# Performance work log

Measured on AMD Instinct MI355X. Metric: run time of the kernel, lower is better.

## Reference

```python
import jax, jax.numpy as jnp
import numpy as np

B, T, D = 8, 1024, 1024

def setup_inputs() -> dict:
    key = jax.random.key(0)
    ks = jax.random.split(key, 9)
    s = D ** -0.5
    return {
        "x": jax.random.normal(ks[0], (B, T, D), dtype=jnp.float32),
        "w_q": jax.random.normal(ks[1], (D, D), dtype=jnp.float32) * s,
        "b_q": jax.random.normal(ks[2], (D,), dtype=jnp.float32) * 0.02,
        "w_k": jax.random.normal(ks[3], (D, D), dtype=jnp.float32) * s,
        "b_k": jax.random.normal(ks[4], (D,), dtype=jnp.float32) * 0.02,
        "w_v": jax.random.normal(ks[5], (D, D), dtype=jnp.float32) * s,
        "b_v": jax.random.normal(ks[6], (D,), dtype=jnp.float32) * 0.02,
        "w_o": jax.random.normal(ks[7], (D, D), dtype=jnp.float32) * s,
        "b_o": jax.random.normal(ks[8], (D,), dtype=jnp.float32) * 0.02,
    }

def reference(x, w_q, b_q, w_k, b_k, w_v, b_v, w_o, b_o):
    d = x.shape[-1]
    scale = jnp.asarray(d, x.dtype) ** -0.5
    q = jnp.einsum('btd,ed->bte', x, w_q) + b_q  # nn.Linear: x @ W^T + b
    k = jnp.einsum('btd,ed->bte', x, w_k) + b_k
    v = jnp.einsum('btd,ed->bte', x, w_v) + b_v
    t = x.shape[1]
    causal = jnp.tril(jnp.ones((t, t), dtype=bool))  # (T, T)
    scores = jnp.einsum('bqd,bkd->bqk', q, k) * scale
    scores = jnp.where(causal, scores, -jnp.inf)
    attn = jax.nn.softmax(scores, axis=-1)  # max-subtraction folded in
    out = jnp.einsum('bqk,bkd->bqd', attn, v)
    return jnp.einsum('btd,ed->bte', out, w_o) + b_o
```

## Files before the change

### kernel.cpp

```cpp
#include <hip/hip_runtime.h>

typedef unsigned short u16;
typedef __attribute__((ext_vector_type(8))) short short8;
typedef __attribute__((ext_vector_type(4))) float f32x4;


__device__ __forceinline__ u16 f2bf(float f) {
  unsigned u = __builtin_bit_cast(unsigned, f);
  u += 0x7fffu + ((u >> 16) & 1u);
  return (u16)(u >> 16);
}

__device__ __forceinline__ void gload16(const void* g, void* l) {
  __builtin_amdgcn_global_load_lds(
      (const __attribute__((address_space(1))) unsigned*)g,
      (__attribute__((address_space(3))) unsigned*)l, 16, 0, 0);
}


#define QTILE(CUR, NXT, DOSTAGE, VM)                                         \
  {                                                                          \
    char* cA = sA0 + (CUR) * 32768;                                          \
    char* cB = sB0 + (CUR) * 16384;                                          \
    short8 bf[2][4], af[2][2];                                               \
                         \
    _Pragma("unroll") for (int kk = 0; kk < 2; ++kk)                         \
      _Pragma("unroll") for (int j = 0; j < 4; ++j) {                        \
        const int rn = wc + j * 16 + l16;                                    \
        bf[kk][j] = *(const short8*)(cB + rn * 128 + (((kk << 2) + quad) ^ (rn & 7)) * 16); \
      }                                                                      \
    _Pragma("unroll") for (int kk = 0; kk < 2; ++kk)                         \
      _Pragma("unroll") for (int i = 0; i < 2; ++i) {                        \
        const int rm = wr + i * 16 + l16;                                    \
        af[kk][i] = *(const short8*)(cA + rm * 128 + (((kk << 2) + quad) ^ (rm & 7)) * 16); \
      }                                                                      \
    if (DOSTAGE) {                                                           \
      char* dA = sA0 + (NXT) * 32768;                                        \
      _Pragma("unroll") for (int j = 0; j < 3; ++j) { gload16(ga[j], dA + la[j]); ga[j] += 64; } \
    }                                                                        \
    asm volatile("" ::: "memory");                                           \
    __builtin_amdgcn_s_barrier();                                            \
    asm volatile("s_waitcnt lgkmcnt(0)" ::: "memory");                       \
    __builtin_amdgcn_sched_barrier(0);                                       \
    __builtin_amdgcn_s_setprio(1);                                           \
    _Pragma("unroll") for (int kk = 0; kk < 2; ++kk)                         \
      _Pragma("unroll") for (int i = 0; i < 2; ++i)                          \
        _Pragma("unroll") for (int j = 0; j < 4; ++j)                        \
          acc[i][j] = __builtin_amdgcn_mfma_f32_16x16x32_bf16(af[kk][i], bf[kk][j], acc[i][j], 0, 0, 0); \
    __builtin_amdgcn_s_setprio(0);                                           \
    asm volatile("" ::: "memory");                                           \
    __builtin_amdgcn_s_barrier();                                            \
    asm volatile("" ::: "memory");                                           \
                                \
    _Pragma("unroll") for (int kk = 0; kk < 2; ++kk)                         \
      _Pragma("unroll") for (int i = 0; i < 2; ++i) {                        \
        const int rm = wr + 32 + i * 16 + l16;                               \
        af[kk][i] = *(const short8*)(cA + rm * 128 + (((kk << 2) + quad) ^ (rm & 7)) * 16); \
      }                                                                      \
    if (DOSTAGE) {                                                           \
      char* dA = sA0 + (NXT) * 32768;                                        \
      char* dB = sB0 + (NXT) * 16384;                                        \
      gload16(ga[3], dA + la[3]); ga[3] += 64;                               \
      _Pragma("unroll") for (int j = 0; j < 2; ++j) { gload16(gb[j], dB + lb[j]); gb[j] += 64; } \
    }                                                                        \
    asm volatile("s_waitcnt vmcnt(" #VM ")" ::: "memory");                   \
    asm volatile("" ::: "memory");                                           \
    __builtin_amdgcn_s_barrier();                                            \
    asm volatile("s_waitcnt lgkmcnt(0)" ::: "memory");                       \
    __builtin_amdgcn_sched_barrier(0);                                       \
    __builtin_amdgcn_s_setprio(1);                                           \
    _Pragma("unroll") for (int kk = 0; kk < 2; ++kk)                         \
      _Pragma("unroll") for (int i = 0; i < 2; ++i)                          \
        _Pragma("unroll") for (int j = 0; j < 4; ++j)                        \
          acc[2 + i][j] = __builtin_amdgcn_mfma_f32_16x16x32_bf16(af[kk][i], bf[kk][j], acc[2 + i][j], 0, 0, 0); \
    __builtin_amdgcn_s_setprio(0);                                           \
    asm volatile("" ::: "memory");                                           \
    __builtin_amdgcn_s_barrier();                                            \
    asm volatile("" ::: "memory");                                           \
  }

__device__ __forceinline__ void gemm_256x128(
    const u16* __restrict__ A, const u16* __restrict__ B,
    int m0, int n0, char* smem, f32x4 acc[4][4])
{
  const int tid  = threadIdx.x;
  const int lane = tid & 63;
  const int quad = lane >> 4;
  const int l16  = lane & 15;
  const int wave = tid >> 6;
  const int wr   = (wave >> 1) << 6;
  const int wc   = (wave & 1) << 6;

  const u16* ga[4]; int la[4];
  const u16* gb[2]; int lb[2];
#pragma unroll
  for (int j = 0; j < 4; ++j) {
    const int L = j * 512 + tid;
    const int r = L >> 3;
    const int c = (L & 7) ^ (r & 7);
    la[j] = L * 16;
    ga[j] = A + (size_t)(m0 + r) * 1024 + c * 8;
  }
#pragma unroll
  for (int j = 0; j < 2; ++j) {
    const int L = j * 512 + tid;
    const int r = L >> 3;
    const int c = (L & 7) ^ (r & 7);
    lb[j] = L * 16;
    gb[j] = B + (size_t)(n0 + r) * 1024 + c * 8;
  }
  char* const sA0 = smem;
  char* const sB0 = smem + 98304;

  {
    char* dA = sA0; char* dB = sB0;
#pragma unroll
    for (int j = 0; j < 4; ++j) { gload16(ga[j], dA + la[j]); ga[j] += 64; }
#pragma unroll
    for (int j = 0; j < 2; ++j) { gload16(gb[j], dB + lb[j]); gb[j] += 64; }
  }
  {
    char* dA = sA0 + 32768; char* dB = sB0 + 16384;
#pragma unroll
    for (int j = 0; j < 4; ++j) { gload16(ga[j], dA + la[j]); ga[j] += 64; }
#pragma unroll
    for (int j = 0; j < 2; ++j) { gload16(gb[j], dB + lb[j]); gb[j] += 64; }
  }
  asm volatile("s_waitcnt vmcnt(6)" ::: "memory");
  __builtin_amdgcn_s_barrier();
  asm volatile("" ::: "memory");

  int cur = 0;
#pragma unroll 1
  for (int t = 0; t < 14; ++t) {
    int nxt = cur + 2; if (nxt >= 3) nxt -= 3;
    QTILE(cur, nxt, true, 6);
    cur = (cur + 1 == 3) ? 0 : cur + 1;
  }
  QTILE(cur, 0, false, 0);
  cur = (cur + 1 == 3) ? 0 : cur + 1;
  QTILE(cur, 0, false, 0);
}

#define ACC_ZERO4(acc) { _Pragma("unroll") for (int i=0;i<4;++i) \
  _Pragma("unroll") for (int j=0;j<4;++j) \
  _Pragma("unroll") for (int r=0;r<4;++r) acc[i][j][r]=0.f; }
#define ACC_ZERO2(acc) { _Pragma("unroll") for (int i=0;i<2;++i) \
  _Pragma("unroll") for (int j=0;j<4;++j) \
  _Pragma("unroll") for (int r=0;r<4;++r) acc[i][j][r]=0.f; }

__device__ __forceinline__ void store256x128_bf16(
    f32x4 acc[4][4], const float* bias, int n0,
    u16* C, int m0, char* smem)
{
  const int tid = threadIdx.x, lane = tid & 63, wave = tid >> 6;
  const int quad = lane >> 4, l16 = lane & 15;
  const int wr = (wave >> 1) << 6, wc = (wave & 1) << 6;
  u16* t = (u16*)smem;
#pragma unroll
  for (int j = 0; j < 4; ++j) {
    const int nn = wc + j * 16 + l16;
    const float bj = bias[n0 + nn];
#pragma unroll
    for (int i = 0; i < 4; ++i) {
      const int mm = wr + i * 16 + quad * 4;
#pragma unroll
      for (int r = 0; r < 4; ++r)
        t[(mm + r) * 136 + nn] = f2bf(acc[i][j][r] + bj);
    }
  }
  __syncthreads();
#pragma unroll
  for (int it = 0; it < 8; ++it) {
    const int L = it * 512 + tid;
    const int mm = L >> 4, cc = L & 15;
    *(uint4*)(C + (size_t)(m0 + mm) * 1024 + n0 + cc * 8) =
        *(const uint4*)(t + mm * 136 + cc * 8);
  }
}

__device__ __forceinline__ void gemm_tile_64(
    const u16* __restrict__ A, int lda,
    const u16* __restrict__ B, int ldb,
    int m0, int n0, int kend,
    char* sA, char* sB, f32x4 acc[2][4])
{
  const int tid  = threadIdx.x;
  const int lane = tid & 63;
  const int wave = tid >> 6;
  const int quad = lane >> 4;
  const int l16  = lane & 15;
  const int wr   = (wave >> 1) << 5;
  const int wc   = (wave & 1) << 6;

  const u16* ga[2]; int la[2];
  const u16* gb[4]; int lb[4];
#pragma unroll
  for (int j = 0; j < 2; ++j) {
    const int Lb = j * 256 + wave * 64;
    const int L  = Lb + lane;
    const int r  = L >> 3;
    const int c  = (L & 7) ^ (r & 7);
    la[j] = Lb * 16;
    ga[j] = A + (size_t)(m0 + r) * lda + c * 8;
  }
#pragma unroll
  for (int j = 0; j < 4; ++j) {
    const int Lb = j * 256 + wave * 64;
    const int L  = Lb + lane;
    const int r  = L >> 3;
    const int c  = (L & 7) ^ (r & 7);
    lb[j] = Lb * 16;
    gb[j] = B + (size_t)(n0 + r) * ldb + c * 8;
  }

  for (int kt = 0; kt < kend; kt += 64) {
#pragma unroll
    for (int j = 0; j < 2; ++j) { gload16(ga[j], sA + la[j]); ga[j] += 64; }
#pragma unroll
    for (int j = 0; j < 4; ++j) { gload16(gb[j], sB + lb[j]); gb[j] += 64; }
    __syncthreads();
#pragma unroll
    for (int kk = 0; kk < 2; ++kk) {
      short8 af[2], bfr[4];
#pragma unroll
      for (int i = 0; i < 2; ++i) {
        const int rm = wr + i * 16 + l16;
        af[i] = *(const short8*)(sA + rm * 128 + (((kk << 2) + quad) ^ (rm & 7)) * 16);
      }
#pragma unroll
      for (int j = 0; j < 4; ++j) {
        const int rn = wc + j * 16 + l16;
        bfr[j] = *(const short8*)(sB + rn * 128 + (((kk << 2) + quad) ^ (rn & 7)) * 16);
      }
#pragma unroll
      for (int i = 0; i < 2; ++i)
#pragma unroll
        for (int j = 0; j < 4; ++j)
          acc[i][j] = __builtin_amdgcn_mfma_f32_16x16x32_bf16(af[i], bfr[j], acc[i][j], 0, 0, 0);
    }
    __syncthreads();
  }
}

__global__ __launch_bounds__(256) void cast_inputs(
    const float* __restrict__ x,  const float* __restrict__ wq,
    const float* __restrict__ wk, const float* __restrict__ wv,
    const float* __restrict__ wo,
    u16* xb, u16* wqb, u16* wkb, u16* wvb, u16* wob, float* rsum)
{
  int b = blockIdx.x;
  if (b < 8) {
    float4 z = {0.f, 0.f, 0.f, 0.f};
    *(float4*)(rsum + (b * 256 + threadIdx.x) * 4) = z;
  }
  const float* src; u16* dst; int base;
  if (b < 4096) { src = x; dst = xb; base = b * 2048; }
  else {
    int r = (b - 4096) >> 9, bb = (b - 4096) & 511;
    base = bb * 2048;
    src = (r == 0) ? wq : (r == 1) ? wk : (r == 2) ? wv : wo;
    dst = (r == 0) ? wqb : (r == 1) ? wkb : (r == 2) ? wvb : wob;
  }
  int i0 = base + threadIdx.x * 8;
  float4 f0 = *(const float4*)(src + i0);
  float4 f1 = *(const float4*)(src + i0 + 4);
  short8 o;
  o[0]=(short)f2bf(f0.x); o[1]=(short)f2bf(f0.y); o[2]=(short)f2bf(f0.z); o[3]=(short)f2bf(f0.w);
  o[4]=(short)f2bf(f1.x); o[5]=(short)f2bf(f1.y); o[6]=(short)f2bf(f1.z); o[7]=(short)f2bf(f1.w);
  *(short8*)(dst + i0) = o;
}

__global__ __launch_bounds__(512, 2) void proj_qkv(
    const u16* __restrict__ xb,
    const u16* __restrict__ wqb, const u16* __restrict__ wkb, const u16* __restrict__ wvb,
    const float* __restrict__ bq, const float* __restrict__ bk, const float* __restrict__ bv,
    u16* q, u16* k, u16* vt)
{
  __shared__ char smem[147456];
  const int z = blockIdx.y;
  const u16* W = (z == 0) ? wqb : (z == 1) ? wkb : wvb;
  const float* bias = (z == 0) ? bq : (z == 1) ? bk : bv;
  const int id = blockIdx.x;
  const int m0 = ((id & 7) * 4 + ((id >> 3) & 3)) * 256;
  const int n0 = (id >> 5) * 128;

  f32x4 acc[4][4]; ACC_ZERO4(acc);
  gemm_256x128(xb, W, m0, n0, smem, acc);

  if (z < 2) {
    store256x128_bf16(acc, bias, n0, (z == 0) ? q : k, m0, smem);
  } else {
    const int tid = threadIdx.x, lane = tid & 63, wave = tid >> 6;
    const int quad = lane >> 4, l16 = lane & 15;
    const int wr = (wave >> 1) << 6, wc = (wave & 1) << 6;
    u16* t = (u16*)smem;
#pragma unroll
    for (int j = 0; j < 4; ++j) {
      const int nn = wc + j * 16 + l16;
      const float bj = bias[n0 + nn];
#pragma unroll
      for (int i = 0; i < 4; ++i) {
        const int mm = wr + i * 16 + quad * 4;
#pragma unroll
        for (int r = 0; r < 4; ++r)
          t[nn * 264 + mm + r] = f2bf(acc[i][j][r] + bj);
      }
    }
    __syncthreads();
    const int b = m0 >> 10, t0 = m0 & 1023;
#pragma unroll
    for (int it = 0; it < 8; ++it) {
      const int L = it * 512 + tid;
      const int nn = L >> 5, cc = L & 31;
      *(uint4*)(vt + ((size_t)b << 20) + (size_t)(n0 + nn) * 1024 + t0 + cc * 8) =
          *(const uint4*)(t + nn * 264 + cc * 8);
    }
  }
}

__global__ __launch_bounds__(256) void qk_expscores(
    const u16* __restrict__ q, const u16* __restrict__ k,
    u16* __restrict__ probs, float* __restrict__ rowsum)
{
  const int id = blockIdx.x;
  const int b = id / 72, t = id - b * 72;
  int p = (int)((__builtin_sqrtf((float)(4 * t + 1)) - 1.f) * 0.5f);
  while ((p + 1) * (p + 2) <= t) ++p;
  while (p * (p + 1) > t) --p;
  int r0 = t - p * (p + 1);
  const int qi = 2 * p + (r0 >= p + 1);
  const int kb = (r0 >= p + 1) ? r0 - (p + 1) : r0;

  __shared__ char smem[24576];
  char* sA = smem; char* sB = smem + 8192;
  const u16* A = q + ((size_t)b << 20);
  const u16* B = k + ((size_t)b << 20);
  const int m0 = qi * 64, n0 = kb * 128;

  f32x4 acc[2][4]; ACC_ZERO2(acc);
  gemm_tile_64(A, 1024, B, 1024, m0, n0, 1024, sA, sB, acc);

  const int tid = threadIdx.x, lane = tid & 63, wave = tid >> 6;
  const int quad = lane >> 4, l16 = lane & 15;
  const int wr = (wave >> 1) << 5, wc = (wave & 1) << 6;
  const bool diag = (kb == (qi >> 1));

  float part[2][4];
#pragma unroll
  for (int i = 0; i < 2; ++i)
#pragma unroll
    for (int r = 0; r < 4; ++r) part[i][r] = 0.f;

  u16* tl = (u16*)smem;
#pragma unroll
  for (int j = 0; j < 4; ++j) {
    const int nn = wc + j * 16 + l16;
#pragma unroll
    for (int i = 0; i < 2; ++i) {
      const int mm = wr + i * 16 + quad * 4;
#pragma unroll
      for (int r = 0; r < 4; ++r) {
        float e = __expf(acc[i][j][r] * 0.03125f);
        if (diag && (n0 + nn) > (m0 + mm + r)) e = 0.f;
        part[i][r] += e;
        tl[(mm + r) * 136 + nn] = f2bf(e);
      }
    }
  }
  float* rs = rowsum + b * 1024 + m0;
#pragma unroll
  for (int i = 0; i < 2; ++i)
#pragma unroll
    for (int r = 0; r < 4; ++r) {
      float v = part[i][r];
      v += __shfl_xor(v, 1); v += __shfl_xor(v, 2);
      v += __shfl_xor(v, 4); v += __shfl_xor(v, 8);
      if (l16 == 0) atomicAdd(rs + wr + i * 16 + quad * 4 + r, v);
    }
  __syncthreads();
  u16* C = probs + ((size_t)b << 20);
#pragma unroll
  for (int it = 0; it < 4; ++it) {
    const int L = it * 256 + tid;
    const int mm = L >> 4, cc = L & 15;
    *(uint4*)(C + (size_t)(m0 + mm) * 1024 + n0 + cc * 8) =
        *(const uint4*)(tl + mm * 136 + cc * 8);
  }
}

__global__ __launch_bounds__(256) void pv_gemm(
    const u16* __restrict__ probs, const u16* __restrict__ vt,
    const float* __restrict__ rowsum, u16* __restrict__ o)
{
  const int id = blockIdx.x;
  const int b = id & 7, nb = (id >> 3) & 7, qi = 15 - (id >> 6);
  __shared__ char smem[24576];
  char* sA = smem; char* sB = smem + 8192;
  const u16* A = probs + ((size_t)b << 20);
  const u16* B = vt + ((size_t)b << 20);
  const int m0 = qi * 64, n0 = nb * 128;
  const int kend = (qi + 1) * 64;

  f32x4 acc[2][4]; ACC_ZERO2(acc);
  gemm_tile_64(A, 1024, B, 1024, m0, n0, kend, sA, sB, acc);

  const int tid = threadIdx.x, lane = tid & 63, wave = tid >> 6;
  const int quad = lane >> 4, l16 = lane & 15;
  const int wr = (wave >> 1) << 5, wc = (wave & 1) << 6;
  const float* rs = rowsum + b * 1024 + m0;
  u16* tl = (u16*)smem;
#pragma unroll
  for (int i = 0; i < 2; ++i)
#pragma unroll
    for (int r = 0; r < 4; ++r) {
      const int mm = wr + i * 16 + quad * 4 + r;
      const float inv = 1.0f / rs[mm];
#pragma unroll
      for (int j = 0; j < 4; ++j)
        tl[mm * 136 + wc + j * 16 + l16] = f2bf(acc[i][j][r] * inv);
    }
  __syncthreads();
  u16* C = o + ((size_t)b << 20);
#pragma unroll
  for (int it = 0; it < 4; ++it) {
    const int L = it * 256 + tid;
    const int mm = L >> 4, cc = L & 15;
    *(uint4*)(C + (size_t)(m0 + mm) * 1024 + n0 + cc * 8) =
        *(const uint4*)(tl + mm * 136 + cc * 8);
  }
}

__global__ __launch_bounds__(512, 2) void proj_o(
    const u16* __restrict__ ob, const u16* __restrict__ wob,
    const float* __restrict__ bo, float* __restrict__ out)
{
  __shared__ char smem[147456];
  const int id = blockIdx.x;
  const int m0 = ((id & 7) * 4 + ((id >> 3) & 3)) * 256;
  const int n0 = (id >> 5) * 128;
  f32x4 acc[4][4]; ACC_ZERO4(acc);
  gemm_256x128(ob, wob, m0, n0, smem, acc);

  const int tid = threadIdx.x, lane = tid & 63, wave = tid >> 6;
  const int quad = lane >> 4, l16 = lane & 15;
  const int wr = (wave >> 1) << 6, wc = (wave & 1) << 6;
  float* tf = (float*)smem;
#pragma unroll
  for (int j = 0; j < 4; ++j) {
    const int nn = wc + j * 16 + l16;
    const float bj = bo[n0 + nn];
#pragma unroll
    for (int i = 0; i < 4; ++i)
#pragma unroll
      for (int r = 0; r < 4; ++r)
        tf[(wr + i * 16 + quad * 4 + r) * 132 + nn] = acc[i][j][r] + bj;
  }
  __syncthreads();
#pragma unroll
  for (int it = 0; it < 16; ++it) {
    const int L = it * 512 + tid;
    const int mm = L >> 5, cc = L & 31;
    *(float4*)(out + (size_t)(m0 + mm) * 1024 + n0 + cc * 4) =
        *(const float4*)(tf + mm * 132 + cc * 4);
  }
}

extern "C" void kernel_launch(void* const* d_in, const int* in_sizes, int n_in,
                              void* d_out, int out_size, void* d_ws, size_t ws_size,
                              hipStream_t stream) {
  const float* x  = (const float*)d_in[0];
  const float* wq = (const float*)d_in[1];
  const float* bq = (const float*)d_in[2];
  const float* wk = (const float*)d_in[3];
  const float* bk = (const float*)d_in[4];
  const float* wv = (const float*)d_in[5];
  const float* bv = (const float*)d_in[6];
  const float* wo = (const float*)d_in[7];
  const float* bo = (const float*)d_in[8];
  float* out = (float*)d_out;

  char* ws = (char*)d_ws;
  const size_t MB = 1u << 20;
  u16*  xb  = (u16*)(ws);
  u16*  wqb = (u16*)(ws + 16*MB);
  u16*  wkb = (u16*)(ws + 18*MB);
  u16*  wvb = (u16*)(ws + 20*MB);
  u16*  wob = (u16*)(ws + 22*MB);
  u16*  qb  = (u16*)(ws + 24*MB);
  u16*  kb  = (u16*)(ws + 40*MB);
  u16*  vtb = (u16*)(ws + 56*MB);
  u16*  pr  = (u16*)(ws + 72*MB);
  float* rsum = (float*)(ws + 88*MB);

  cast_inputs<<<6144, 256, 0, stream>>>(x, wq, wk, wv, wo, xb, wqb, wkb, wvb, wob, rsum);
  proj_qkv<<<dim3(256, 3), 512, 0, stream>>>(xb, wqb, wkb, wvb, bq, bk, bv, qb, kb, vtb);
  qk_expscores<<<576, 256, 0, stream>>>(qb, kb, pr, rsum);
  pv_gemm<<<1024, 256, 0, stream>>>(pr, vtb, rsum, xb );
  proj_o<<<256, 512, 0, stream>>>(xb, wob, bo, out);
}
```

Measured before the change: 234.1 us.

## Software-pipeline LDS fragment loads across GEMM k-tiles with register double-buffering

Restructures the 256x128 GEMM main loop so that B and A0 fragments for the next k-tile are read from LDS during the current tile, using two ping-pong B register sets. This cuts the per-tile barriers from four to one and overlaps LDS reads with MFMA work. The LDS layout also moves to interleaved A/B stages of 48KB each. In exchange it raises register pressure and relies on a carefully ordered waitcnt and barrier sequence, plus an extra __syncthreads at the end.

```diff
diff --git a/kernel.cpp b/kernel.cpp
--- a/kernel.cpp
+++ b/kernel.cpp
@@ -18,65 +18,69 @@
 }
 
 
-#define QTILE(CUR, NXT, DOSTAGE, VM)                                         \
-  {                                                                          \
-    char* cA = sA0 + (CUR) * 32768;                                          \
-    char* cB = sB0 + (CUR) * 16384;                                          \
-    short8 bf[2][4], af[2][2];                                               \
-                         \
-    _Pragma("unroll") for (int kk = 0; kk < 2; ++kk)                         \
-      _Pragma("unroll") for (int j = 0; j < 4; ++j) {                        \
-        const int rn = wc + j * 16 + l16;                                    \
-        bf[kk][j] = *(const short8*)(cB + rn * 128 + (((kk << 2) + quad) ^ (rn & 7)) * 16); \
-      }                                                                      \
-    _Pragma("unroll") for (int kk = 0; kk < 2; ++kk)                         \
-      _Pragma("unroll") for (int i = 0; i < 2; ++i) {                        \
-        const int rm = wr + i * 16 + l16;                                    \
-        af[kk][i] = *(const short8*)(cA + rm * 128 + (((kk << 2) + quad) ^ (rm & 7)) * 16); \
-      }                                                                      \
-    if (DOSTAGE) {                                                           \
-      char* dA = sA0 + (NXT) * 32768;                                        \
-      _Pragma("unroll") for (int j = 0; j < 3; ++j) { gload16(ga[j], dA + la[j]); ga[j] += 64; } \
-    }                                                                        \
-    asm volatile("" ::: "memory");                                           \
-    __builtin_amdgcn_s_barrier();                                            \
-    asm volatile("s_waitcnt lgkmcnt(0)" ::: "memory");                       \
-    __builtin_amdgcn_sched_barrier(0);                                       \
-    __builtin_amdgcn_s_setprio(1);                                           \
-    _Pragma("unroll") for (int kk = 0; kk < 2; ++kk)                         \
-      _Pragma("unroll") for (int i = 0; i < 2; ++i)                          \
-        _Pragma("unroll") for (int j = 0; j < 4; ++j)                        \
-          acc[i][j] = __builtin_amdgcn_mfma_f32_16x16x32_bf16(af[kk][i], bf[kk][j], acc[i][j], 0, 0, 0); \
-    __builtin_amdgcn_s_setprio(0);                                           \
-    asm volatile("" ::: "memory");                                           \
-    __builtin_amdgcn_s_barrier();                                            \
-    asm volatile("" ::: "memory");                                           \
-                                \
-    _Pragma("unroll") for (int kk = 0; kk < 2; ++kk)                         \
-      _Pragma("unroll") for (int i = 0; i < 2; ++i) {                        \
-        const int rm = wr + 32 + i * 16 + l16;                               \
-        af[kk][i] = *(const short8*)(cA + rm * 128 + (((kk << 2) + quad) ^ (rm & 7)) * 16); \
-      }                                                                      \
-    if (DOSTAGE) {                                                           \
-      char* dA = sA0 + (NXT) * 32768;                                        \
-      char* dB = sB0 + (NXT) * 16384;                                        \
-      gload16(ga[3], dA + la[3]); ga[3] += 64;                               \
-      _Pragma("unroll") for (int j = 0; j < 2; ++j) { gload16(gb[j], dB + lb[j]); gb[j] += 64; } \
-    }                                                                        \
-    asm volatile("s_waitcnt vmcnt(" #VM ")" ::: "memory");                   \
-    asm volatile("" ::: "memory");                                           \
-    __builtin_amdgcn_s_barrier();                                            \
-    asm volatile("s_waitcnt lgkmcnt(0)" ::: "memory");                       \
-    __builtin_amdgcn_sched_barrier(0);                                       \
-    __builtin_amdgcn_s_setprio(1);                                           \
-    _Pragma("unroll") for (int kk = 0; kk < 2; ++kk)                         \
-      _Pragma("unroll") for (int i = 0; i < 2; ++i)                          \
-        _Pragma("unroll") for (int j = 0; j < 4; ++j)                        \
-          acc[2 + i][j] = __builtin_amdgcn_mfma_f32_16x16x32_bf16(af[kk][i], bf[kk][j], acc[2 + i][j], 0, 0, 0); \
-    __builtin_amdgcn_s_setprio(0);                                           \
-    asm volatile("" ::: "memory");                                           \
-    __builtin_amdgcn_s_barrier();                                            \
-    asm volatile("" ::: "memory");                                           \
+#define PTILE(RB_C, RB_N, DOSTAGE, VM, LAST)                                  \
+  {                                                                           \
+    char* cA = sA0 + cur * 49152;                                             \
+                                                       \
+    if (DOSTAGE) {                                                            \
+      const int ns = (cur + 2 >= 3) ? cur - 1 : cur + 2;                      \
+      char* dA = sA0 + ns * 49152;                                            \
+      _Pragma("unroll") for (int j = 0; j < 3; ++j) {                         \
+        gload16(ga[j], dA + la[j]); ga[j] += 64; }                            \
+    }                                                                         \
+    _Pragma("unroll") for (int kk = 0; kk < 2; ++kk)                          \
+      _Pragma("unroll") for (int i = 0; i < 2; ++i) {                         \
+        const int rm = wr + 32 + i * 16 + l16;                                \
+        a1f[kk][i] = *(const short8*)(cA + rm * 128 +                         \
+            (((kk << 2) + quad) ^ (rm & 7)) * 16);                            \
+      }                                                                       \
+    asm volatile("s_waitcnt lgkmcnt(4)" ::: "memory");                        \
+    __builtin_amdgcn_sched_barrier(0);                                        \
+    __builtin_amdgcn_s_setprio(1);                                            \
+    _Pragma("unroll") for (int kk = 0; kk < 2; ++kk)                          \
+      _Pragma("unroll") for (int i = 0; i < 2; ++i)                           \
+        _Pragma("unroll") for (int j = 0; j < 4; ++j)                         \
+          acc[i][j] = __builtin_amdgcn_mfma_f32_16x16x32_bf16(                \
+              a0f[kk][i], RB_C[kk][j], acc[i][j], 0, 0, 0);                   \
+    __builtin_amdgcn_s_setprio(0);                                            \
+                                                       \
+    if (DOSTAGE) {                                                            \
+      const int ns = (cur + 2 >= 3) ? cur - 1 : cur + 2;                      \
+      char* dA = sA0 + ns * 49152; char* dB = dA + 32768;                     \
+      gload16(ga[3], dA + la[3]); ga[3] += 64;                                \
+      _Pragma("unroll") for (int j = 0; j < 2; ++j) {                         \
+        gload16(gb[j], dB + lb[j]); gb[j] += 64; }                            \
+    }                                                                         \
+    if (!(LAST)) {                                                            \
+      asm volatile("s_waitcnt vmcnt(" #VM ") lgkmcnt(0)" ::: "memory");       \
+      __builtin_amdgcn_s_barrier();                                           \
+      asm volatile("" ::: "memory");                                          \
+      const int nc = (cur + 1 >= 3) ? 0 : cur + 1;                            \
+      char* nA = sA0 + nc * 49152; char* nB = nA + 32768;                     \
+      _Pragma("unroll") for (int kk = 0; kk < 2; ++kk)                        \
+        _Pragma("unroll") for (int j = 0; j < 4; ++j) {                       \
+          const int rn = wc + j * 16 + l16;                                   \
+          RB_N[kk][j] = *(const short8*)(nB + rn * 128 +                      \
+              (((kk << 2) + quad) ^ (rn & 7)) * 16);                          \
+        }                                                                     \
+      _Pragma("unroll") for (int kk = 0; kk < 2; ++kk)                        \
+        _Pragma("unroll") for (int i = 0; i < 2; ++i) {                       \
+          const int rm = wr + i * 16 + l16;                                   \
+          a0f[kk][i] = *(const short8*)(nA + rm * 128 +                       \
+              (((kk << 2) + quad) ^ (rm & 7)) * 16);                          \
+        }                                                                     \
+    } else {                                                                  \
+      asm volatile("s_waitcnt lgkmcnt(0)" ::: "memory");                      \
+    }                                                                         \
+    __builtin_amdgcn_sched_barrier(0);                                        \
+    __builtin_amdgcn_s_setprio(1);                                            \
+    _Pragma("unroll") for (int kk = 0; kk < 2; ++kk)                          \
+      _Pragma("unroll") for (int i = 0; i < 2; ++i)                           \
+        _Pragma("unroll") for (int j = 0; j < 4; ++j)                         \
+          acc[2 + i][j] = __builtin_amdgcn_mfma_f32_16x16x32_bf16(            \
+              a1f[kk][i], RB_C[kk][j], acc[2 + i][j], 0, 0, 0);               \
+    __builtin_amdgcn_s_setprio(0);                                            \
+    cur = (cur + 1 >= 3) ? 0 : cur + 1;                                       \
   }
 
 __device__ __forceinline__ void gemm_256x128(
@@ -110,17 +114,17 @@
     gb[j] = B + (size_t)(n0 + r) * 1024 + c * 8;
   }
   char* const sA0 = smem;
-  char* const sB0 = smem + 98304;
+
+  short8 bfr0[2][4], bfr1[2][4];
+  short8 a0f[2][2], a1f[2][2];
 
   {
-    char* dA = sA0; char* dB = sB0;
+    char* dA = sA0; char* dB = sA0 + 32768;
 #pragma unroll
     for (int j = 0; j < 4; ++j) { gload16(ga[j], dA + la[j]); ga[j] += 64; }
 #pragma unroll
     for (int j = 0; j < 2; ++j) { gload16(gb[j], dB + lb[j]); gb[j] += 64; }
-  }
-  {
-    char* dA = sA0 + 32768; char* dB = sB0 + 16384;
+    dA = sA0 + 49152; dB = dA + 32768;
 #pragma unroll
     for (int j = 0; j < 4; ++j) { gload16(ga[j], dA + la[j]); ga[j] += 64; }
 #pragma unroll
@@ -129,17 +133,33 @@
   asm volatile("s_waitcnt vmcnt(6)" ::: "memory");
   __builtin_amdgcn_s_barrier();
   asm volatile("" ::: "memory");
+  {
+    char* nA = sA0; char* nB = sA0 + 32768;
+#pragma unroll
+    for (int kk = 0; kk < 2; ++kk)
+#pragma unroll
+      for (int j = 0; j < 4; ++j) {
+        const int rn = wc + j * 16 + l16;
+        bfr0[kk][j] = *(const short8*)(nB + rn * 128 + (((kk << 2) + quad) ^ (rn & 7)) * 16);
+      }
+#pragma unroll
+    for (int kk = 0; kk < 2; ++kk)
+#pragma unroll
+      for (int i = 0; i < 2; ++i) {
+        const int rm = wr + i * 16 + l16;
+        a0f[kk][i] = *(const short8*)(nA + rm * 128 + (((kk << 2) + quad) ^ (rm & 7)) * 16);
+      }
+  }
 
   int cur = 0;
 #pragma unroll 1
-  for (int t = 0; t < 14; ++t) {
-    int nxt = cur + 2; if (nxt >= 3) nxt -= 3;
-    QTILE(cur, nxt, true, 6);
-    cur = (cur + 1 == 3) ? 0 : cur + 1;
-  }
-  QTILE(cur, 0, false, 0);
-  cur = (cur + 1 == 3) ? 0 : cur + 1;
-  QTILE(cur, 0, false, 0);
+  for (int it = 0; it < 7; ++it) {
+    PTILE(bfr0, bfr1, true, 6, false);
+    PTILE(bfr1, bfr0, true, 6, false);
+  }
+  PTILE(bfr0, bfr1, false, 0, false);
+  PTILE(bfr1, bfr0, false, 0, true);
+  __syncthreads();
 }
 
 #define ACC_ZERO4(acc) { _Pragma("unroll") for (int i=0;i<4;++i) \
```

Measured after the change: 225.9 us. -3.5%, faster.
